# Optimization experiments

Measured on AMD Instinct MI355X. Metric: run time of the kernel, lower is better.

Reference implementation:

```python
import jax, jax.numpy as jnp
import numpy as np

EPS = 1e-10
PHI = (1.0 + np.sqrt(5.0)) / 2.0
TAU = 2.0 * np.pi
LOG_CUTOFF = float(np.log(PHI ** 2))  # log(lambda_cutoff)


def _log_abs_diff(la, lb, same_sign):
    # log|a - b| (same sign) or log(|a| + |b|) (opposite sign), all in log space
    hi = jnp.maximum(la, lb)
    lo = jnp.minimum(la, lb)
    d = jnp.minimum(lo - hi, -1e-7)  # guard log1p(-1) on the (masked) diagonal
    log_diff = hi + jnp.log1p(-jnp.exp(d))
    log_sum = jnp.logaddexp(la, lb)
    return jnp.where(same_sign, log_diff, log_sum)


def log_cartesian_distance(ell1, theta1, ell2, theta2):
    # elementwise / broadcasting version of compute_log_cartesian_distance
    cos1, sin1 = jnp.cos(theta1), jnp.sin(theta1)
    cos2, sin2 = jnp.cos(theta2), jnp.sin(theta2)
    lx1 = ell1 + jnp.log(jnp.abs(cos1) + EPS)
    ly1 = ell1 + jnp.log(jnp.abs(sin1) + EPS)
    lx2 = ell2 + jnp.log(jnp.abs(cos2) + EPS)
    ly2 = ell2 + jnp.log(jnp.abs(sin2) + EPS)
    same_x = (jnp.sign(cos1) * jnp.sign(cos2)) > 0
    same_y = (jnp.sign(sin1) * jnp.sign(sin2)) > 0
    ldx = _log_abs_diff(lx1, lx2, same_x)
    ldy = _log_abs_diff(ly1, ly2, same_y)
    # 0.5 * logsumexp(2*ldx, 2*ldy) == log sqrt(dx^2 + dy^2)
    return 0.5 * jnp.logaddexp(2.0 * ldx, 2.0 * ldy)


def setup_inputs() -> dict:
    N = 4096
    key = jax.random.key(0)
    k1, k2 = jax.random.split(key)
    ell = jax.random.uniform(k1, (N,), dtype=jnp.float32) * np.float32(np.log(PHI ** 3))
    theta = jax.random.uniform(k2, (N,), dtype=jnp.float32) * np.float32(TAU)
    s = jnp.ones((N,), dtype=jnp.float32)
    frozen = jnp.zeros((N,), dtype=bool)
    return {"ell": ell, "theta": theta, "s": s, "frozen": frozen}


def reference(ell, theta, s, frozen):
    # compute_repulsion_direct: all-pairs log-distance repulsion with phi^2 cutoff
    N = ell.shape[0]
    # pairwise log distances: [N, N]
    ld = log_cartesian_distance(ell[:, None], theta[:, None], ell[None, :], theta[None, :])
    pair_mask = (ld <= LOG_CUTOFF) & (~jnp.eye(N, dtype=bool)) & (~frozen)[:, None]
    force = s[:, None] * s[None, :] * jnp.exp(-ld)  # s_i * s_j / dist
    force = jnp.where(pair_mask, force, jnp.zeros((), force.dtype))
    d_theta = jnp.mod(theta[None, :] - theta[:, None] + np.float32(np.pi), np.float32(TAU)) - np.float32(np.pi)
    d_ell = ell[None, :] - ell[:, None]
    F_ell = jnp.sum(force * d_ell, axis=1)
    F_theta = jnp.sum(force * d_theta, axis=1)
    return jnp.stack([F_ell, F_theta])  # [2, N]
```

## Files before the change

### kernel.cpp

```cpp
#include <hip/hip_runtime.h>
#include <math.h>

#define BLOCK 256
#define CHUNK 64

#define PI_F      3.14159265358979323846f
#define TAU_F     6.2831853071795864769f
#define INV_TAU_F 0.15915494309189533577f
#define PHI4_F    6.854101966249685f

__global__ void precompute_kernel(const float* __restrict__ ell,
                                  const float* __restrict__ theta,
                                  float4* __restrict__ A, int n) {
    int i = blockIdx.x * blockDim.x + threadIdx.x;
    if (i < n) {
        float e = ell[i];
        float th = theta[i];
        float lam = expf(e);
        float sn, cs;
        sincosf(th, &sn, &cs);
        A[i] = make_float4(lam * cs, lam * sn, e, th);
    }
}

__global__ __launch_bounds__(BLOCK) void repulse_kernel(
        const float4* __restrict__ A,
        const float* __restrict__ s,
        const unsigned char* __restrict__ frozen,
        float* __restrict__ out, int n) {
    int i = blockIdx.x * BLOCK + threadIdx.x;
    if (i >= n) return;
    int j0 = blockIdx.y * CHUNK;

    float4 a = A[i];
    float si = s[i];
    float xi = a.x, yi = a.y, eli = a.z;
    float api = PI_F - a.w;

    float Fe = 0.0f, Ft = 0.0f;

    int jend = j0 + CHUNK;
    if (jend > n) jend = n;

#pragma unroll 8
    for (int j = j0; j < jend; ++j) {
        float4 b = A[j];
        float sj = s[j];
        float dx = b.x - xi;
        float dy = b.y - yi;
        float r2 = fmaf(dx, dx, dy * dy);
        float f = si * sj * rsqrtf(fmaxf(r2, 1e-30f));
        bool ok = (r2 <= PHI4_F) && (j != i);
        f = ok ? f : 0.0f;
        float t = b.w + api;
        float dth = fmaf(-floorf(t * INV_TAU_F), TAU_F, t) - PI_F;
        Fe = fmaf(f, b.z - eli, Fe);
        Ft = fmaf(f, dth, Ft);
    }

    if (frozen[i]) { Fe = 0.0f; Ft = 0.0f; }
    atomicAdd(&out[i], Fe);
    atomicAdd(&out[n + i], Ft);
}

extern "C" void kernel_launch(void* const* d_in, const int* in_sizes, int n_in,
                              void* d_out, int out_size, void* d_ws, size_t ws_size,
                              hipStream_t stream) {
    const float* ell   = (const float*)d_in[0];
    const float* theta = (const float*)d_in[1];
    const float* s     = (const float*)d_in[2];
    const unsigned char* frozen = (const unsigned char*)d_in[3];
    float* out = (float*)d_out;
    int n = in_sizes[0];

    float4* A = (float4*)d_ws;

    hipMemsetAsync(d_out, 0, (size_t)out_size * sizeof(float), stream);

    int pre_blocks = (n + BLOCK - 1) / BLOCK;
    precompute_kernel<<<pre_blocks, BLOCK, 0, stream>>>(ell, theta, A, n);

    dim3 grid((n + BLOCK - 1) / BLOCK, (n + CHUNK - 1) / CHUNK);
    repulse_kernel<<<grid, BLOCK, 0, stream>>>(A, s, frozen, out, n);
}
```

Measured before the change: 71.85 us.

## Restructure repulsion to block-per-i-group with j-strided threads and wave reductions

Each block now handles 4 target particles, and its threads stride over all j, so the per-j loads are shared across 4 i values held in registers. Per-block sums are built with wave shuffles plus a shared-memory reduction and written directly, which removes the atomics and the output memset. It also swaps rsqrtf for the raw hardware rsq builtin and factors s[i] out of the inner loop. In exchange there is reduction overhead, and there is no bounds check for i when n is not a multiple of 4.

```diff
diff --git a/kernel.cpp b/kernel.cpp
--- a/kernel.cpp
+++ b/kernel.cpp
@@ -2,12 +2,14 @@
 #include <math.h>
 
 #define BLOCK 256
-#define CHUNK 64
+#define IPB 4
 
 #define PI_F      3.14159265358979323846f
 #define TAU_F     6.2831853071795864769f
 #define INV_TAU_F 0.15915494309189533577f
 #define PHI4_F    6.854101966249685f
+
+extern "C" __device__ float __builtin_amdgcn_rsqf(float);
 
 __global__ void precompute_kernel(const float* __restrict__ ell,
                                   const float* __restrict__ theta,
@@ -28,39 +30,75 @@
         const float* __restrict__ s,
         const unsigned char* __restrict__ frozen,
         float* __restrict__ out, int n) {
-    int i = blockIdx.x * BLOCK + threadIdx.x;
-    if (i >= n) return;
-    int j0 = blockIdx.y * CHUNK;
+    const int t  = threadIdx.x;
+    const int i0 = blockIdx.x * IPB;
 
-    float4 a = A[i];
-    float si = s[i];
-    float xi = a.x, yi = a.y, eli = a.z;
-    float api = PI_F - a.w;
+    float xi[IPB], yi[IPB], eli[IPB], api[IPB];
+    int   iv[IPB];
+#pragma unroll
+    for (int v = 0; v < IPB; ++v) {
+        int i = i0 + v;
+        iv[v] = i;
+        float4 a = A[i];
+        xi[v] = a.x; yi[v] = a.y; eli[v] = a.z;
+        api[v] = PI_F - a.w;
+    }
 
-    float Fe = 0.0f, Ft = 0.0f;
+    float Fe[IPB], Ft[IPB];
+#pragma unroll
+    for (int v = 0; v < IPB; ++v) { Fe[v] = 0.0f; Ft[v] = 0.0f; }
 
-    int jend = j0 + CHUNK;
-    if (jend > n) jend = n;
-
-#pragma unroll 8
-    for (int j = j0; j < jend; ++j) {
+#pragma unroll 4
+    for (int j = t; j < n; j += BLOCK) {
         float4 b = A[j];
         float sj = s[j];
-        float dx = b.x - xi;
-        float dy = b.y - yi;
-        float r2 = fmaf(dx, dx, dy * dy);
-        float f = si * sj * rsqrtf(fmaxf(r2, 1e-30f));
-        bool ok = (r2 <= PHI4_F) && (j != i);
-        f = ok ? f : 0.0f;
-        float t = b.w + api;
-        float dth = fmaf(-floorf(t * INV_TAU_F), TAU_F, t) - PI_F;
-        Fe = fmaf(f, b.z - eli, Fe);
-        Ft = fmaf(f, dth, Ft);
+#pragma unroll
+        for (int v = 0; v < IPB; ++v) {
+            float dx = b.x - xi[v];
+            float dy = b.y - yi[v];
+            float r2 = fmaf(dx, dx, dy * dy);
+            float rinv = __builtin_amdgcn_rsqf(fmaxf(r2, 1e-30f));
+            bool ok = (r2 <= PHI4_F) && (j != iv[v]);
+            float f = ok ? sj * rinv : 0.0f;
+            float tt = b.w + api[v];
+            float dth = fmaf(-floorf(tt * INV_TAU_F), TAU_F, tt) - PI_F;
+            Fe[v] = fmaf(f, b.z - eli[v], Fe[v]);
+            Ft[v] = fmaf(f, dth, Ft[v]);
+        }
     }
 
-    if (frozen[i]) { Fe = 0.0f; Ft = 0.0f; }
-    atomicAdd(&out[i], Fe);
-    atomicAdd(&out[n + i], Ft);
+#pragma unroll
+    for (int v = 0; v < IPB; ++v) {
+#pragma unroll
+        for (int off = 32; off >= 1; off >>= 1) {
+            Fe[v] += __shfl_xor(Fe[v], off, 64);
+            Ft[v] += __shfl_xor(Ft[v], off, 64);
+        }
+    }
+
+    __shared__ float red[(BLOCK / 64) * IPB * 2];
+    const int wave = t >> 6;
+    const int lane = t & 63;
+    if (lane == 0) {
+#pragma unroll
+        for (int v = 0; v < IPB; ++v) {
+            red[wave * IPB * 2 + v * 2 + 0] = Fe[v];
+            red[wave * IPB * 2 + v * 2 + 1] = Ft[v];
+        }
+    }
+    __syncthreads();
+
+    if (t < IPB * 2) {
+        int v  = t >> 1;
+        int c  = t & 1;
+        float sum = 0.0f;
+#pragma unroll
+        for (int w = 0; w < BLOCK / 64; ++w)
+            sum += red[w * IPB * 2 + v * 2 + c];
+        int i = i0 + v;
+        float val = frozen[i] ? 0.0f : s[i] * sum;
+        out[c * n + i] = val;
+    }
 }
 
 extern "C" void kernel_launch(void* const* d_in, const int* in_sizes, int n_in,
@@ -75,11 +113,9 @@
 
     float4* A = (float4*)d_ws;
 
-    hipMemsetAsync(d_out, 0, (size_t)out_size * sizeof(float), stream);
-
     int pre_blocks = (n + BLOCK - 1) / BLOCK;
     precompute_kernel<<<pre_blocks, BLOCK, 0, stream>>>(ell, theta, A, n);
 
-    dim3 grid((n + BLOCK - 1) / BLOCK, (n + CHUNK - 1) / CHUNK);
+    int grid = (n + IPB - 1) / IPB;
     repulse_kernel<<<grid, BLOCK, 0, stream>>>(A, s, frozen, out, n);
 }
```

After: 69.84 us. -2.8%, faster.
